# Kernel tuning notes

Hardware: AMD Instinct MI355X
Metric: run time of the kernel (lower is better)

## Reference

```python
import jax, jax.numpy as jnp
import numpy as np

HEAD_DIM = 128
N_HEADS = 32
N_KV_HEADS = 8
EPS = 1e-6
ROPE_THETA = 1e6
NEG_INF = -1e9


def _rms_norm(x, w):
    # per-head RMSNorm over last dim (head_dim), fp32 math like Qwen3RMSNorm
    xf = x.astype(jnp.float32)
    var = jnp.mean(xf * xf, axis=-1, keepdims=True)
    return (w * (xf * jax.lax.rsqrt(var + EPS))).astype(x.dtype)


def _rope_cos_sin(position_ids, dtype):
    # default rope: inv_freq = theta^(-2i/d), emb = cat(freqs, freqs)
    inv_freq = 1.0 / (ROPE_THETA ** (jnp.arange(0, HEAD_DIM, 2, dtype=jnp.float32) / HEAD_DIM))
    freqs = position_ids.astype(jnp.float32)[:, :, None] * inv_freq[None, None, :]  # [B,S,hd/2]
    emb = jnp.concatenate([freqs, freqs], axis=-1)  # [B,S,hd]
    return jnp.cos(emb).astype(dtype), jnp.sin(emb).astype(dtype)


def _rotate_half(x):
    x1, x2 = jnp.split(x, 2, axis=-1)
    return jnp.concatenate([-x2, x1], axis=-1)


def setup_inputs() -> dict:
    key = jax.random.key(0)
    ks = jax.random.split(key, 6)
    B, S, H = 1, 2048, 4096
    return {
        "hidden_states": jax.random.normal(ks[0], (B, S, H), jnp.float32),
        "position_ids": jnp.broadcast_to(jnp.arange(S, dtype=jnp.int32)[None, :], (B, S)),
        "Wq": jax.random.normal(ks[1], (N_HEADS * HEAD_DIM, H), jnp.float32) * 0.02,
        "Wk": jax.random.normal(ks[2], (N_KV_HEADS * HEAD_DIM, H), jnp.float32) * 0.02,
        "Wv": jax.random.normal(ks[3], (N_KV_HEADS * HEAD_DIM, H), jnp.float32) * 0.02,
        "Wo": jax.random.normal(ks[4], (H, N_HEADS * HEAD_DIM), jnp.float32) * 0.02,
        "q_norm_w": jnp.ones((HEAD_DIM,), jnp.float32),
        "k_norm_w": jnp.ones((HEAD_DIM,), jnp.float32),
    }


def reference(hidden_states, position_ids, Wq, Wk, Wv, Wo, q_norm_w, k_norm_w):
    B, S, H = hidden_states.shape
    scaling = HEAD_DIM ** -0.5
    n_rep = N_HEADS // N_KV_HEADS

    # projections (torch Linear: y = x @ W.T), reshape to [B, heads, S, hd]
    q = jnp.einsum('bsh,dh->bsd', hidden_states, Wq).reshape(B, S, N_HEADS, HEAD_DIM)
    k = jnp.einsum('bsh,dh->bsd', hidden_states, Wk).reshape(B, S, N_KV_HEADS, HEAD_DIM)
    v = jnp.einsum('bsh,dh->bsd', hidden_states, Wv).reshape(B, S, N_KV_HEADS, HEAD_DIM)

    q = _rms_norm(q, q_norm_w).transpose(0, 2, 1, 3)  # [B,nH,S,hd]
    k = _rms_norm(k, k_norm_w).transpose(0, 2, 1, 3)  # [B,nKV,S,hd]
    v = v.transpose(0, 2, 1, 3)

    cos, sin = _rope_cos_sin(position_ids, hidden_states.dtype)
    cos = cos[:, None, :, :]  # unsqueeze head dim
    sin = sin[:, None, :, :]
    q = q * cos + _rotate_half(q) * sin
    k = k * cos + _rotate_half(k) * sin

    # GQA repeat_kv
    k = jnp.repeat(k, n_rep, axis=1)
    v = jnp.repeat(v, n_rep, axis=1)

    scores = jnp.einsum('bhqd,bhkd->bhqk', q, k) * scaling
    causal = jnp.where(
        jnp.arange(S)[:, None] >= jnp.arange(S)[None, :], 0.0, NEG_INF
    ).astype(scores.dtype)
    scores = scores + causal[None, None, :, :]
    attn = jax.nn.softmax(scores.astype(jnp.float32), axis=-1).astype(q.dtype)

    out = jnp.einsum('bhqk,bhkd->bhqd', attn, v)
    out = out.transpose(0, 2, 1, 3).reshape(B, S, N_HEADS * HEAD_DIM)
    return jnp.einsum('bsd,hd->bsh', out, Wo)
```

## Files before the change

### kernel.cpp

```cpp
#include <hip/hip_runtime.h>
#include <hip/hip_bf16.h>

typedef unsigned short u16;
typedef __bf16 bf16x8 __attribute__((ext_vector_type(8)));
typedef u16 u16x4 __attribute__((ext_vector_type(4)));
typedef u16 u16x8 __attribute__((ext_vector_type(8)));
typedef float f32x4 __attribute__((ext_vector_type(4)));

#define S_LEN  2048
#define HID    4096
#define NHEADS 32
#define NKV    8
#define HD     128
#define QDIM   (NHEADS*HD)
#define KVDIM  (NKV*HD)
#define NT     (S_LEN/64)

__device__ __forceinline__ u16 f2bf(float f) {
  unsigned u = __float_as_uint(f);
  u += 0x7fff + ((u >> 16) & 1);
  return (u16)(u >> 16);
}
__device__ __forceinline__ void lds_load16(const u16* g, u16* l) {
  __builtin_amdgcn_global_load_lds(
      (__attribute__((address_space(1))) void*)(g),
      (__attribute__((address_space(3))) void*)(l), 16, 0, 0);
}

__global__ __launch_bounds__(256) void f2b4(
    const float* __restrict__ s0, u16* __restrict__ d0, long n0,
    const float* __restrict__ s1, u16* __restrict__ d1, long n1,
    const float* __restrict__ s2, u16* __restrict__ d2, long n2,
    const float* __restrict__ s3, u16* __restrict__ d3, long n3)
{
  const float* s; u16* d; long n; int b0, nb;
  const int b = blockIdx.x;
  if (b < 1024)      { s=s0; d=d0; n=n0; b0=0;    nb=1024; }
  else if (b < 3072) { s=s1; d=d1; n=n1; b0=1024; nb=2048; }
  else if (b < 3584) { s=s2; d=d2; n=n2; b0=3072; nb=512;  }
  else               { s=s3; d=d3; n=n3; b0=3584; nb=512;  }
  long i = (long)(b - b0)*256 + threadIdx.x;
  const long stride = (long)nb*256;
  for (; i < n; i += stride) {
    f32x4 a = ((const f32x4*)s)[i*2];
    f32x4 c = ((const f32x4*)s)[i*2 + 1];
    u16x8 o;
    #pragma unroll
    for (int j = 0; j < 4; ++j) { o[j] = f2bf(a[j]); o[4+j] = f2bf(c[j]); }
    ((u16x8*)d)[i] = o;
  }
}

__global__ __launch_bounds__(256) void f2b(
    const float* __restrict__ in, u16* __restrict__ out, long n8)
{
  long i = (long)blockIdx.x * blockDim.x + threadIdx.x;
  const long stride = (long)gridDim.x * blockDim.x;
  for (; i < n8; i += stride) {
    f32x4 a = ((const f32x4*)in)[i*2];
    f32x4 b = ((const f32x4*)in)[i*2 + 1];
    u16x8 o;
    #pragma unroll
    for (int j = 0; j < 4; ++j) { o[j] = f2bf(a[j]); o[4+j] = f2bf(b[j]); }
    ((u16x8*)out)[i] = o;
  }
}

__global__ __launch_bounds__(512, 2) void gemmQ(
    const u16* __restrict__ A, const u16* __restrict__ B,
    u16* __restrict__ Cq, u16* __restrict__ Ck, u16* __restrict__ Cv,
    int K)
{
  __shared__ u16 lds[57344];
  const int tid  = threadIdx.x;
  const int lane = tid & 63;
  const int w    = tid >> 6;
  const int wr   = w >> 2, wc = w & 3;
  const int l16  = lane & 15, lhi = lane >> 4;
  const long arow0 = (long)blockIdx.y * 256;
  const long brow0 = (long)blockIdx.x * 192;
  const int ntiles = K >> 6;

  const int cu = ((lane & 7) ^ (lane >> 3)) * 8;
  const int wl = w*8 + (lane >> 3);
  const u16* Ag[4];
  #pragma unroll
  for (int r = 0; r < 4; ++r)
    Ag[r] = A + (arow0 + r*64 + wl)*(long)K + cu;
  const u16* Bg[3];
  #pragma unroll
  for (int r = 0; r < 2; ++r) {
    const int rp = r*64 + wl;
    Bg[r] = B + (brow0 + (rp >> 5)*48 + (rp & 31))*(long)K + cu;
  }
  Bg[2] = B + (brow0 + (wl >> 4)*48 + 32 + (wl & 15))*(long)K + cu;

  auto stageA = [&](int s, int kt) {
    u16* d = lds + ((kt & 1) << 14) + w*512;
    lds_load16(Ag[s]   + (long)kt*64, d + s*4096);
    lds_load16(Ag[s+2] + (long)kt*64, d + (s+2)*4096);
  };
  auto stageB0 = [&](int kt) {
    u16* d = lds + 32768 + (kt & 1)*12288 + w*512;
    lds_load16(Bg[0] + (long)kt*64, d);
    lds_load16(Bg[1] + (long)kt*64, d + 4096);
  };
  auto stageB1 = [&](int kt) {
    u16* d = lds + 32768 + (kt & 1)*12288 + w*512;
    lds_load16(Bg[2] + (long)kt*64, d + 8192);
  };

  const int xr = (l16 & 7) << 3;
  int offA[4][2], offB[2][2], offB2[2];
  #pragma unroll
  for (int m2 = 0; m2 < 4; ++m2)
    #pragma unroll
    for (int ks = 0; ks < 2; ++ks)
      offA[m2][ks] = (wr*128 + m2*16 + l16)*64 + ((ks*32 + lhi*8) ^ xr);
  #pragma unroll
  for (int n2 = 0; n2 < 2; ++n2)
    #pragma unroll
    for (int ks = 0; ks < 2; ++ks)
      offB[n2][ks] = (wc*32 + n2*16 + l16)*64 + ((ks*32 + lhi*8) ^ xr);
  #pragma unroll
  for (int ks = 0; ks < 2; ++ks)
    offB2[ks] = 8192 + (wc*16 + l16)*64 + ((ks*32 + lhi*8) ^ xr);

  f32x4 acc[8][3] = {};

  stageA(0, 0); stageB0(0); stageB1(0); stageA(1, 0);
  stageA(0, 1); stageB0(1); stageB1(1);
  asm volatile("s_waitcnt vmcnt(5)" ::: "memory");
  __builtin_amdgcn_s_barrier();

  #pragma unroll 2
  for (int t = 0; t < ntiles; ++t) {
    const int Ab = (t & 1) << 14;
    const int Bb = 32768 + (t & 1)*12288;
    bf16x8 af[4][2], af2[4][2], bf[2][2], bf2[2];

    #pragma unroll
    for (int m2 = 0; m2 < 4; ++m2)
      #pragma unroll
      for (int ks = 0; ks < 2; ++ks)
        af[m2][ks] = *(const bf16x8*)(lds + Ab + offA[m2][ks]);
    #pragma unroll
    for (int n2 = 0; n2 < 2; ++n2)
      #pragma unroll
      for (int ks = 0; ks < 2; ++ks)
        bf[n2][ks] = *(const bf16x8*)(lds + Bb + offB[n2][ks]);
    if (t + 1 < ntiles) stageA(1, t + 1);
    __builtin_amdgcn_s_barrier();
    asm volatile("s_waitcnt lgkmcnt(0)" ::: "memory");
    __builtin_amdgcn_s_setprio(1);
    #pragma unroll
    for (int m2 = 0; m2 < 4; ++m2)
      #pragma unroll
      for (int n2 = 0; n2 < 2; ++n2)
        #pragma unroll
        for (int ks = 0; ks < 2; ++ks)
          acc[m2][n2] = __builtin_amdgcn_mfma_f32_16x16x32_bf16(
              af[m2][ks], bf[n2][ks], acc[m2][n2], 0, 0, 0);
    __builtin_amdgcn_s_setprio(0);
    __builtin_amdgcn_s_barrier();

    #pragma unroll
    for (int ks = 0; ks < 2; ++ks)
      bf2[ks] = *(const bf16x8*)(lds + Bb + offB2[ks]);
    if (t + 2 < ntiles) stageA(0, t + 2);
    __builtin_amdgcn_s_barrier();
    asm volatile("s_waitcnt lgkmcnt(0)" ::: "memory");
    __builtin_amdgcn_s_setprio(1);
    #pragma unroll
    for (int m2 = 0; m2 < 4; ++m2)
      #pragma unroll
      for (int ks = 0; ks < 2; ++ks)
        acc[m2][2] = __builtin_amdgcn_mfma_f32_16x16x32_bf16(
            af[m2][ks], bf2[ks], acc[m2][2], 0, 0, 0);
    __builtin_amdgcn_s_setprio(0);
    __builtin_amdgcn_s_barrier();

    #pragma unroll
    for (int m2 = 0; m2 < 4; ++m2)
      #pragma unroll
      for (int ks = 0; ks < 2; ++ks)
        af2[m2][ks] = *(const bf16x8*)(lds + Ab + 4096 + offA[m2][ks]);
    if (t + 2 < ntiles) stageB0(t + 2);
    __builtin_amdgcn_s_barrier();
    asm volatile("s_waitcnt lgkmcnt(0)" ::: "memory");
    __builtin_amdgcn_s_setprio(1);
    #pragma unroll
    for (int m2 = 0; m2 < 4; ++m2)
      #pragma unroll
      for (int ks = 0; ks < 2; ++ks)
        acc[4+m2][2] = __builtin_amdgcn_mfma_f32_16x16x32_bf16(
            af2[m2][ks], bf2[ks], acc[4+m2][2], 0, 0, 0);
    __builtin_amdgcn_s_setprio(0);
    __builtin_amdgcn_s_barrier();

    if (t + 2 < ntiles) stageB1(t + 2);
    __builtin_amdgcn_s_barrier();
    __builtin_amdgcn_s_setprio(1);
    #pragma unroll
    for (int m2 = 0; m2 < 4; ++m2)
      #pragma unroll
      for (int n2 = 0; n2 < 2; ++n2)
        #pragma unroll
        for (int ks = 0; ks < 2; ++ks)
          acc[4+m2][n2] = __builtin_amdgcn_mfma_f32_16x16x32_bf16(
              af2[m2][ks], bf[n2][ks], acc[4+m2][n2], 0, 0, 0);
    __builtin_amdgcn_s_setprio(0);
    if (t + 2 < ntiles) { asm volatile("s_waitcnt vmcnt(5)" ::: "memory"); }
    else                { asm volatile("s_waitcnt vmcnt(0)" ::: "memory"); }
    __builtin_amdgcn_s_barrier();
  }

  #pragma unroll
  for (int m = 0; m < 8; ++m) {
    const long row = arow0 + wr*128 + (m >> 2)*64 + (m & 3)*16 + lhi*4;
    #pragma unroll
    for (int n = 0; n < 3; ++n) {
      const long col = brow0 + wc*48 + n*16 + l16;
      if (col < QDIM) {
        #pragma unroll
        for (int r = 0; r < 4; ++r)
          Cq[(row + r)*QDIM + col] = f2bf(acc[m][n][r]);
      } else if (col < QDIM + KVDIM) {
        #pragma unroll
        for (int r = 0; r < 4; ++r)
          Ck[(row + r)*KVDIM + (col - QDIM)] = f2bf(acc[m][n][r]);
      } else {
        u16x4 o;
        #pragma unroll
        for (int r = 0; r < 4; ++r) o[r] = f2bf(acc[m][n][r]);
        *(u16x4*)(Cv + (col - QDIM - KVDIM)*(long)S_LEN + row) = o;
      }
    }
  }
}

__global__ __launch_bounds__(512, 2) void gemmF(
    const u16* __restrict__ A, const u16* __restrict__ B,
    float* __restrict__ C, int M, int N, int K)
{
  __shared__ u16 lds[49152];
  const int tid  = threadIdx.x;
  const int lane = tid & 63;
  const int w    = tid >> 6;
  const int wr   = w >> 2, wc = w & 3;
  const int l16  = lane & 15, lhi = lane >> 4;
  const long arow0 = (long)blockIdx.y * 128;
  const long brow0 = (long)blockIdx.x * 256;
  const int ntiles = K >> 6;

  const int cu = ((lane & 7) ^ (lane >> 3)) * 8;
  const int rA  = (w >> 2)*64 + (w & 3)*8;
  const int rB1c = 128 + (w >> 2)*64 + (w & 3)*8;
  const u16* srcA  = A + (arow0 + rA   + (lane >> 3))*(long)K + cu;
  const u16* srcB0 = B + (brow0 + rA   + (lane >> 3))*(long)K + cu;
  const u16* srcB1 = B + (brow0 + rB1c + (lane >> 3))*(long)K + cu;
  u16* const dA  = lds + rA*64;
  u16* const dB0 = lds + 16384 + rA*64;
  u16* const dB1 = lds + 16384 + rB1c*64;

  auto stageA = [&](int s, int kt) {
    lds_load16(srcA + (long)(s*32)*K + kt*64,
               dA + ((kt & 1) << 13) + s*2048);
  };
  auto stageB = [&](int s, int kt) {
    const long so = (long)(s*32)*K + kt*64;
    const int  d  = ((kt & 1) << 14) + s*2048;
    lds_load16(srcB0 + so, dB0 + d);
    lds_load16(srcB1 + so, dB1 + d);
  };

  const int xr = (l16 & 7) << 3;
  int offA[2][2], offB[2][2];
  #pragma unroll
  for (int m = 0; m < 2; ++m)
    #pragma unroll
    for (int ks = 0; ks < 2; ++ks)
      offA[m][ks] = (wr*64 + m*16 + l16)*64 + ((ks*32 + lhi*8) ^ xr);
  #pragma unroll
  for (int n = 0; n < 2; ++n)
    #pragma unroll
    for (int ks = 0; ks < 2; ++ks)
      offB[n][ks] = (wc*64 + n*16 + l16)*64 + ((ks*32 + lhi*8) ^ xr);

  f32x4 acc[4][4] = {};

  stageA(0, 0); stageA(1, 0); stageB(0, 0); stageB(1, 0);
  if (ntiles > 1) { stageA(0, 1); stageB(0, 1); stageB(1, 1); }
  asm volatile("s_waitcnt vmcnt(5)" ::: "memory");
  __builtin_amdgcn_s_barrier();

  #pragma unroll 2
  for (int t = 0; t < ntiles; ++t) {
    const int Ab = (t & 1) << 13;
    const int Bb = 16384 + ((t & 1) << 14);
    bf16x8 af[2][2], bf[2][2], af2[2][2], bf2[2][2];

    #pragma unroll
    for (int m = 0; m < 2; ++m)
      #pragma unroll
      for (int ks = 0; ks < 2; ++ks)
        af[m][ks] = *(const bf16x8*)(lds + Ab + offA[m][ks]);
    #pragma unroll
    for (int n = 0; n < 2; ++n)
      #pragma unroll
      for (int ks = 0; ks < 2; ++ks)
        bf[n][ks] = *(const bf16x8*)(lds + Bb + offB[n][ks]);
    if (t + 1 < ntiles) stageA(1, t + 1);
    __builtin_amdgcn_s_barrier();
    asm volatile("s_waitcnt lgkmcnt(0)" ::: "memory");
    __builtin_amdgcn_s_setprio(1);
    #pragma unroll
    for (int m = 0; m < 2; ++m)
      #pragma unroll
      for (int n = 0; n < 2; ++n)
        #pragma unroll
        for (int ks = 0; ks < 2; ++ks)
          acc[m][n] = __builtin_amdgcn_mfma_f32_16x16x32_bf16(
              af[m][ks], bf[n][ks], acc[m][n], 0, 0, 0);
    __builtin_amdgcn_s_setprio(0);
    __builtin_amdgcn_s_barrier();

    #pragma unroll
    for (int n = 0; n < 2; ++n)
      #pragma unroll
      for (int ks = 0; ks < 2; ++ks)
        bf2[n][ks] = *(const bf16x8*)(lds + Bb + 2048 + offB[n][ks]);
    if (t + 2 < ntiles) stageA(0, t + 2);
    __builtin_amdgcn_s_barrier();
    asm volatile("s_waitcnt lgkmcnt(0)" ::: "memory");
    __builtin_amdgcn_s_setprio(1);
    #pragma unroll
    for (int m = 0; m < 2; ++m)
      #pragma unroll
      for (int n = 0; n < 2; ++n)
        #pragma unroll
        for (int ks = 0; ks < 2; ++ks)
          acc[m][2+n] = __builtin_amdgcn_mfma_f32_16x16x32_bf16(
              af[m][ks], bf2[n][ks], acc[m][2+n], 0, 0, 0);
    __builtin_amdgcn_s_setprio(0);
    __builtin_amdgcn_s_barrier();

    #pragma unroll
    for (int m = 0; m < 2; ++m)
      #pragma unroll
      for (int ks = 0; ks < 2; ++ks)
        af2[m][ks] = *(const bf16x8*)(lds + Ab + 2048 + offA[m][ks]);
    if (t + 2 < ntiles) stageB(0, t + 2);
    __builtin_amdgcn_s_barrier();
    asm volatile("s_waitcnt lgkmcnt(0)" ::: "memory");
    __builtin_amdgcn_s_setprio(1);
    #pragma unroll
    for (int m = 0; m < 2; ++m)
      #pragma unroll
      for (int n = 0; n < 2; ++n)
        #pragma unroll
        for (int ks = 0; ks < 2; ++ks)
          acc[2+m][2+n] = __builtin_amdgcn_mfma_f32_16x16x32_bf16(
              af2[m][ks], bf2[n][ks], acc[2+m][2+n], 0, 0, 0);
    __builtin_amdgcn_s_setprio(0);
    __builtin_amdgcn_s_barrier();

    if (t + 2 < ntiles) stageB(1, t + 2);
    __builtin_amdgcn_s_barrier();
    __builtin_amdgcn_s_setprio(1);
    #pragma unroll
    for (int m = 0; m < 2; ++m)
      #pragma unroll
      for (int n = 0; n < 2; ++n)
        #pragma unroll
        for (int ks = 0; ks < 2; ++ks)
          acc[2+m][n] = __builtin_amdgcn_mfma_f32_16x16x32_bf16(
              af2[m][ks], bf[n][ks], acc[2+m][n], 0, 0, 0);
    __builtin_amdgcn_s_setprio(0);
    if (t + 2 < ntiles) { asm volatile("s_waitcnt vmcnt(5)" ::: "memory"); }
    else                { asm volatile("s_waitcnt vmcnt(0)" ::: "memory"); }
    __builtin_amdgcn_s_barrier();
  }

  #pragma unroll
  for (int mi = 0; mi < 4; ++mi) {
    const long row = arow0 + wr*64 + (mi >> 1)*32 + (mi & 1)*16 + lhi*4;
    #pragma unroll
    for (int ni = 0; ni < 4; ++ni) {
      const long col = brow0 + wc*64 + (ni >> 1)*32 + (ni & 1)*16 + l16;
      #pragma unroll
      for (int r = 0; r < 4; ++r)
        C[(row + r)*N + col] = acc[mi][ni][r];
    }
  }
}

__global__ __launch_bounds__(256) void norm_rope2(
    u16* __restrict__ Qb, u16* __restrict__ Kb,
    const float* __restrict__ qw, const float* __restrict__ kw,
    const int* __restrict__ pos)
{
  const int row  = blockIdx.x * 4 + (threadIdx.x >> 6);
  const int lane = threadIdx.x & 63;
  u16* p; const float* nw; float sc; int s;
  if (row < S_LEN*NHEADS) {
    p = Qb + (long)row * HD; nw = qw; sc = 0.08838834764831845f; s = row >> 5;
  } else {
    const int r2 = row - S_LEN*NHEADS;
    p = Kb + (long)r2 * HD; nw = kw; sc = 1.0f; s = r2 >> 3;
  }

  float x1 = __uint_as_float(((unsigned)p[lane]) << 16);
  float x2 = __uint_as_float(((unsigned)p[lane + 64]) << 16);
  float ss = x1*x1 + x2*x2;
  #pragma unroll
  for (int m = 32; m >= 1; m >>= 1) ss += __shfl_xor(ss, m);
  const float inv = rsqrtf(ss * (1.0f/128.0f) + 1e-6f);
  x1 *= inv * nw[lane];
  x2 *= inv * nw[lane + 64];

  const float inv_freq = expf(-(float)lane * (13.815510557964274f / 64.0f));
  const float ang = (float)pos[s] * inv_freq;
  float sn, cs;
  sincosf(ang, &sn, &cs);
  p[lane]      = f2bf((x1*cs - x2*sn) * sc);
  p[lane + 64] = f2bf((x2*cs + x1*sn) * sc);
}

__global__ __launch_bounds__(256, 4) void attn(
    const u16* __restrict__ Q, const u16* __restrict__ K,
    const u16* __restrict__ VT, u16* __restrict__ O,
    float* __restrict__ OP0, float* __restrict__ OP1, float* __restrict__ ML)
{
  __shared__ u16 Ks[64*128];
  __shared__ u16 Vt[128*64];
  __shared__ u16 Ps[4*16*64];

  const int tid  = threadIdx.x;
  const int lane = tid & 63;
  const int w    = tid >> 6;
  const int l16  = lane & 15, lhi = lane >> 4;

  const int bx = blockIdx.x;
  int h, Tq, t0, t1;
  bool split;
  if (bx < 1024) {
    const int pid  = bx >> 1;
    const int half = bx & 1;
    Tq = 31 - (pid >> 5);
    h  = pid & 31;
    const int nk = Tq + 1, nh = nk >> 1;
    t0 = half ? nh : 0;
    t1 = half ? nk : nh;
    split = true;
  } else {
    const int s = bx - 1024;
    Tq = 15 - (s >> 5);
    h  = s & 31;
    t0 = 0; t1 = Tq + 1;
    split = false;
  }
  const int kh = h >> 2;
  const int qrow0 = Tq*64 + w*16;

  bf16x8 qf[4];
  #pragma unroll
  for (int ks = 0; ks < 4; ++ks)
    qf[ks] = *(const bf16x8*)(Q + (long)(qrow0 + l16)*QDIM + h*HD + ks*32 + lhi*8);

  float mr[4] = {-1e30f,-1e30f,-1e30f,-1e30f};
  float lr[4] = {0.f,0.f,0.f,0.f};
  f32x4 of[8] = {};
  u16* Pw = Ps + w*16*64;

  for (int t = t0; t < t1; ++t) {
    const int kv0 = t * 64;
    #pragma unroll
    for (int i = 0; i < 4; ++i) {
      const int r   = w*16 + i*4 + lhi;
      const int col = (l16*8) ^ ((r & 7) << 3);
      lds_load16(K + (long)(kv0 + r)*KVDIM + kh*HD + col,
                 Ks + (w*16 + i*4)*128);
    }
    #pragma unroll
    for (int i = 0; i < 4; ++i) {
      const int r   = w*32 + i*8 + (lane >> 3);
      const int col = ((lane & 7)*8) ^ ((r & 7) << 3);
      lds_load16(VT + (long)(kh*HD + r)*S_LEN + kv0 + col,
                 Vt + (w*32 + i*8)*64);
    }
    __syncthreads();

    f32x4 sa[4] = {};
    __builtin_amdgcn_s_setprio(1);
    #pragma unroll
    for (int n = 0; n < 4; ++n)
      #pragma unroll
      for (int ks = 0; ks < 4; ++ks) {
        bf16x8 kf = *(const bf16x8*)(
            Ks + (n*16 + l16)*128 + ((ks*32 + lhi*8) ^ ((l16 & 7) << 3)));
        sa[n] = __builtin_amdgcn_mfma_f32_16x16x32_bf16(qf[ks], kf, sa[n], 0, 0, 0);
      }
    __builtin_amdgcn_s_setprio(0);

    const bool diag = (t == Tq);
    float pm[4];
    #pragma unroll
    for (int r = 0; r < 4; ++r) {
      const int grow = qrow0 + lhi*4 + r;
      #pragma unroll
      for (int n = 0; n < 4; ++n) {
        float sv = sa[n][r];
        if (diag && (kv0 + n*16 + l16 > grow)) sv = -1e9f;
        sa[n][r] = sv;
      }
      float p01 = fmaxf(sa[0][r], sa[1][r]);
      float p23 = fmaxf(sa[2][r], sa[3][r]);
      float pmx = fmaxf(p01, p23);
      pmx = fmaxf(pmx, __shfl_xor(pmx, 1));
      pmx = fmaxf(pmx, __shfl_xor(pmx, 2));
      pmx = fmaxf(pmx, __shfl_xor(pmx, 4));
      pmx = fmaxf(pmx, __shfl_xor(pmx, 8));
      pm[r] = pmx;
    }
    bool need = (pm[0] > mr[0] + 8.f) | (pm[1] > mr[1] + 8.f) |
                (pm[2] > mr[2] + 8.f) | (pm[3] > mr[3] + 8.f);
    if (__any(need)) {
      #pragma unroll
      for (int r = 0; r < 4; ++r) {
        const float mnew  = fmaxf(mr[r], pm[r]);
        const float alpha = __expf(mr[r] - mnew);
        mr[r] = mnew;
        lr[r] *= alpha;
        #pragma unroll
        for (int c = 0; c < 8; ++c) of[c][r] *= alpha;
      }
    }
    #pragma unroll
    for (int r = 0; r < 4; ++r) {
      float rsum = 0.f;
      #pragma unroll
      for (int n = 0; n < 4; ++n) {
        float pv = __expf(sa[n][r] - mr[r]);
        sa[n][r] = pv;
        rsum += pv;
      }
      rsum += __shfl_xor(rsum, 1);
      rsum += __shfl_xor(rsum, 2);
      rsum += __shfl_xor(rsum, 4);
      rsum += __shfl_xor(rsum, 8);
      lr[r] += rsum;
    }

    #pragma unroll
    for (int r = 0; r < 4; ++r) {
      const int prow = lhi*4 + r;
      #pragma unroll
      for (int n = 0; n < 4; ++n)
        Pw[prow*64 + ((n*16 + l16) ^ ((prow & 7) << 3))] = f2bf(sa[n][r]);
    }
    __builtin_amdgcn_s_setprio(1);
    #pragma unroll
    for (int ks = 0; ks < 2; ++ks) {
      bf16x8 pf = *(const bf16x8*)(
          Pw + l16*64 + ((ks*32 + lhi*8) ^ ((l16 & 7) << 3)));
      #pragma unroll
      for (int c = 0; c < 8; ++c) {
        bf16x8 vf = *(const bf16x8*)(
            Vt + (c*16 + l16)*64 + ((ks*32 + lhi*8) ^ ((l16 & 7) << 3)));
        of[c] = __builtin_amdgcn_mfma_f32_16x16x32_bf16(pf, vf, of[c], 0, 0, 0);
      }
    }
    __builtin_amdgcn_s_setprio(0);
    __syncthreads();
  }

  if (split) {
    float* Op = ((bx & 1) ? OP1 : OP0) + (long)(bx >> 1) * 8192;
    #pragma unroll
    for (int r = 0; r < 4; ++r) {
      const int row = w*16 + lhi*4 + r;
      #pragma unroll
      for (int c = 0; c < 8; ++c)
        Op[row*128 + c*16 + l16] = of[c][r];
      if (l16 == 0) {
        ML[(long)bx*128 + row*2]     = mr[r];
        ML[(long)bx*128 + row*2 + 1] = lr[r];
      }
    }
  } else {
    #pragma unroll
    for (int r = 0; r < 4; ++r) {
      const float invl = 1.0f / lr[r];
      const long orow = (long)(qrow0 + lhi*4 + r) * QDIM + h*HD;
      #pragma unroll
      for (int c = 0; c < 8; ++c)
        O[orow + c*16 + l16] = f2bf(of[c][r] * invl);
    }
  }
}

__global__ __launch_bounds__(256) void mrg(
    const float* __restrict__ OP0, const float* __restrict__ OP1,
    const float* __restrict__ ML, u16* __restrict__ O)
{
  const int r0  = blockIdx.x*2 + (threadIdx.x >> 7);
  const int pid = r0 >> 6;
  const int row = r0 & 63;
  const int d   = threadIdx.x & 127;
  const int Tq  = 31 - (pid >> 5);
  const int h   = pid & 31;
  const long mb0 = (long)(2*pid)*128 + row*2;
  const long mb1 = mb0 + 128;
  const float m0 = ML[mb0],     l0 = ML[mb0 + 1];
  const float m1 = ML[mb1],     l1 = ML[mb1 + 1];
  const float m  = fmaxf(m0, m1);
  const float a0 = __expf(m0 - m), a1 = __expf(m1 - m);
  const float o0 = OP0[(long)pid*8192 + row*128 + d];
  const float o1 = OP1[(long)pid*8192 + row*128 + d];
  const float o  = (o0*a0 + o1*a1) / (l0*a0 + l1*a1);
  O[(long)(Tq*64 + row)*QDIM + h*HD + d] = f2bf(o);
}

extern "C" void kernel_launch(void* const* d_in, const int* in_sizes, int n_in,
                              void* d_out, int out_size, void* d_ws, size_t ws_size,
                              hipStream_t stream) {
  (void)in_sizes; (void)n_in; (void)out_size; (void)ws_size;
  const float* hs  = (const float*)d_in[0];
  const int*   pos = (const int*)d_in[1];
  const float* Wq  = (const float*)d_in[2];
  const float* Wk  = (const float*)d_in[3];
  const float* Wv  = (const float*)d_in[4];
  const float* Wo  = (const float*)d_in[5];
  const float* qw  = (const float*)d_in[6];
  const float* kw  = (const float*)d_in[7];

  u16* hsB = (u16*)d_ws;
  u16* W1  = hsB + (long)S_LEN*HID;
  u16* WkB = W1  + (long)QDIM*HID;
  u16* WvB = WkB + (long)KVDIM*HID;
  u16* Kb  = WvB + (long)KVDIM*HID;
  u16* VT  = Kb  + (long)S_LEN*KVDIM;
  u16* AO  = VT  + (long)KVDIM*S_LEN;
  u16* Qb  = (u16*)d_out;

  float* OP0 = (float*)hsB;
  float* OP1 = (float*)WkB;
  float* ML  = (float*)(Qb + (long)S_LEN*QDIM);

  f2b4<<<4096, 256, 0, stream>>>(hs, hsB, (long)S_LEN*HID/8,
                                 Wq, W1,  (long)QDIM*HID/8,
                                 Wk, WkB, (long)KVDIM*HID/8,
                                 Wv, WvB, (long)KVDIM*HID/8);

  gemmQ<<<dim3((QDIM+2*KVDIM)/192, S_LEN/256), 512, 0, stream>>>(
      hsB, W1, Qb, Kb, VT, HID);

  norm_rope2<<<(S_LEN*NHEADS + S_LEN*NKV)/4, 256, 0, stream>>>(
      Qb, Kb, qw, kw, pos);

  f2b<<<2048, 256, 0, stream>>>(Wo, W1, (long)HID*QDIM/8);

  attn<<<dim3(1536), 256, 0, stream>>>(Qb, Kb, VT, AO, OP0, OP1, ML);
  mrg<<<dim3(16384), 256, 0, stream>>>(OP0, OP1, ML, AO);

  gemmF<<<dim3(HID/256, S_LEN/128), 512, 0, stream>>>(
      AO, W1, (float*)d_out, S_LEN, HID, QDIM);
}
```

Baseline: 361.1 us.

## Balance causal attention work by pairing high and low query tiles per block

After: 348.7 us. 1.04x faster.

```diff
diff --git a/kernel.cpp b/kernel.cpp
--- a/kernel.cpp
+++ b/kernel.cpp
@@ -441,161 +441,158 @@
   const int w    = tid >> 6;
   const int l16  = lane & 15, lhi = lane >> 4;
 
-  const int bx = blockIdx.x;
-  int h, Tq, t0, t1;
-  bool split;
-  if (bx < 1024) {
-    const int pid  = bx >> 1;
-    const int half = bx & 1;
-    Tq = 31 - (pid >> 5);
-    h  = pid & 31;
-    const int nk = Tq + 1, nh = nk >> 1;
-    t0 = half ? nh : 0;
-    t1 = half ? nk : nh;
-    split = true;
-  } else {
-    const int s = bx - 1024;
-    Tq = 15 - (s >> 5);
-    h  = s & 31;
-    t0 = 0; t1 = Tq + 1;
-    split = false;
-  }
-  const int kh = h >> 2;
-  const int qrow0 = Tq*64 + w*16;
-
-  bf16x8 qf[4];
-  #pragma unroll
-  for (int ks = 0; ks < 4; ++ks)
-    qf[ks] = *(const bf16x8*)(Q + (long)(qrow0 + l16)*QDIM + h*HD + ks*32 + lhi*8);
-
-  float mr[4] = {-1e30f,-1e30f,-1e30f,-1e30f};
-  float lr[4] = {0.f,0.f,0.f,0.f};
-  f32x4 of[8] = {};
-  u16* Pw = Ps + w*16*64;
-
-  for (int t = t0; t < t1; ++t) {
-    const int kv0 = t * 64;
-    #pragma unroll
-    for (int i = 0; i < 4; ++i) {
-      const int r   = w*16 + i*4 + lhi;
-      const int col = (l16*8) ^ ((r & 7) << 3);
-      lds_load16(K + (long)(kv0 + r)*KVDIM + kh*HD + col,
-                 Ks + (w*16 + i*4)*128);
+  const int kh   = blockIdx.x & 7;
+  const int idx  = blockIdx.x >> 3;
+  const int cc   = idx & 31;
+  const int jj   = idx >> 5;
+  const int h    = kh*4 + jj;
+  const int k    = cc ^ (jj & 1);
+  const int p    = k >> 1;
+  const int role = k & 1;
+  const int hi   = 31 - p, lo = p;
+  const int pid  = h*16 + p;
+
+  const int nseg = role ? 2 : 1;
+  for (int sg = 0; sg < nseg; ++sg) {
+    const int qt  = sg ? lo : hi;
+    const int tt0 = (sg == 0 && role) ? 16 : 0;
+    const int tt1 = sg ? (lo + 1) : (role ? hi + 1 : 16);
+    const int qrow0 = qt*64 + w*16;
+
+    bf16x8 qf[4];
+    #pragma unroll
+    for (int ks = 0; ks < 4; ++ks)
+      qf[ks] = *(const bf16x8*)(Q + (long)(qrow0 + l16)*QDIM + h*HD + ks*32 + lhi*8);
+
+    float mr[4] = {-1e30f,-1e30f,-1e30f,-1e30f};
+    float lr[4] = {0.f,0.f,0.f,0.f};
+    f32x4 of[8] = {};
+    u16* Pw = Ps + w*16*64;
+
+    for (int t = tt0; t < tt1; ++t) {
+      const int kv0 = t * 64;
+      #pragma unroll
+      for (int i = 0; i < 4; ++i) {
+        const int r   = w*16 + i*4 + lhi;
+        const int col = (l16*8) ^ ((r & 7) << 3);
+        lds_load16(K + (long)(kv0 + r)*KVDIM + kh*HD + col,
+                   Ks + (w*16 + i*4)*128);
+      }
+      #pragma unroll
+      for (int i = 0; i < 4; ++i) {
+        const int r   = w*32 + i*8 + (lane >> 3);
+        const int col = ((lane & 7)*8) ^ ((r & 7) << 3);
+        lds_load16(VT + (long)(kh*HD + r)*S_LEN + kv0 + col,
+                   Vt + (w*32 + i*8)*64);
+      }
+      __syncthreads();
+
+      f32x4 sa[4] = {};
+      __builtin_amdgcn_s_setprio(1);
+      #pragma unroll
+      for (int n = 0; n < 4; ++n)
+        #pragma unroll
+        for (int ks = 0; ks < 4; ++ks) {
+          bf16x8 kf = *(const bf16x8*)(
+              Ks + (n*16 + l16)*128 + ((ks*32 + lhi*8) ^ ((l16 & 7) << 3)));
+          sa[n] = __builtin_amdgcn_mfma_f32_16x16x32_bf16(qf[ks], kf, sa[n], 0, 0, 0);
+        }
+      __builtin_amdgcn_s_setprio(0);
+
+      const bool diag = (t == qt);
+      float pm[4];
+      #pragma unroll
+      for (int r = 0; r < 4; ++r) {
+        const int grow = qrow0 + lhi*4 + r;
+        #pragma unroll
+        for (int n = 0; n < 4; ++n) {
+          float sv = sa[n][r];
+          if (diag && (kv0 + n*16 + l16 > grow)) sv = -1e9f;
+          sa[n][r] = sv;
+        }
+        float p01 = fmaxf(sa[0][r], sa[1][r]);
+        float p23 = fmaxf(sa[2][r], sa[3][r]);
+        float pmx = fmaxf(p01, p23);
+        pmx = fmaxf(pmx, __shfl_xor(pmx, 1));
+        pmx = fmaxf(pmx, __shfl_xor(pmx, 2));
+        pmx = fmaxf(pmx, __shfl_xor(pmx, 4));
+        pmx = fmaxf(pmx, __shfl_xor(pmx, 8));
+        pm[r] = pmx;
+      }
+      bool need = (pm[0] > mr[0] + 8.f) | (pm[1] > mr[1] + 8.f) |
+                  (pm[2] > mr[2] + 8.f) | (pm[3] > mr[3] + 8.f);
+      if (__any(need)) {
+        #pragma unroll
+        for (int r = 0; r < 4; ++r) {
+          const float mnew  = fmaxf(mr[r], pm[r]);
+          const float alpha = __expf(mr[r] - mnew);
+          mr[r] = mnew;
+          lr[r] *= alpha;
+          #pragma unroll
+          for (int c = 0; c < 8; ++c) of[c][r] *= alpha;
+        }
+      }
+      #pragma unroll
+      for (int r = 0; r < 4; ++r) {
+        float rsum = 0.f;
+        #pragma unroll
+        for (int n = 0; n < 4; ++n) {
+          float pv = __expf(sa[n][r] - mr[r]);
+          sa[n][r] = pv;
+          rsum += pv;
+        }
+        rsum += __shfl_xor(rsum, 1);
+        rsum += __shfl_xor(rsum, 2);
+        rsum += __shfl_xor(rsum, 4);
+        rsum += __shfl_xor(rsum, 8);
+        lr[r] += rsum;
+      }
+
+      #pragma unroll
+      for (int r = 0; r < 4; ++r) {
+        const int prow = lhi*4 + r;
+        #pragma unroll
+        for (int n = 0; n < 4; ++n)
+          Pw[prow*64 + ((n*16 + l16) ^ ((prow & 7) << 3))] = f2bf(sa[n][r]);
+      }
+      __builtin_amdgcn_s_setprio(1);
+      #pragma unroll
+      for (int ks = 0; ks < 2; ++ks) {
+        bf16x8 pf = *(const bf16x8*)(
+            Pw + l16*64 + ((ks*32 + lhi*8) ^ ((l16 & 7) << 3)));
+        #pragma unroll
+        for (int c = 0; c < 8; ++c) {
+          bf16x8 vf = *(const bf16x8*)(
+              Vt + (c*16 + l16)*64 + ((ks*32 + lhi*8) ^ ((l16 & 7) << 3)));
+          of[c] = __builtin_amdgcn_mfma_f32_16x16x32_bf16(pf, vf, of[c], 0, 0, 0);
+        }
+      }
+      __builtin_amdgcn_s_setprio(0);
+      __syncthreads();
     }
-    #pragma unroll
-    for (int i = 0; i < 4; ++i) {
-      const int r   = w*32 + i*8 + (lane >> 3);
-      const int col = ((lane & 7)*8) ^ ((r & 7) << 3);
-      lds_load16(VT + (long)(kh*HD + r)*S_LEN + kv0 + col,
-                 Vt + (w*32 + i*8)*64);
-    }
-    __syncthreads();
-
-    f32x4 sa[4] = {};
-    __builtin_amdgcn_s_setprio(1);
-    #pragma unroll
-    for (int n = 0; n < 4; ++n)
-      #pragma unroll
-      for (int ks = 0; ks < 4; ++ks) {
-        bf16x8 kf = *(const bf16x8*)(
-            Ks + (n*16 + l16)*128 + ((ks*32 + lhi*8) ^ ((l16 & 7) << 3)));
-        sa[n] = __builtin_amdgcn_mfma_f32_16x16x32_bf16(qf[ks], kf, sa[n], 0, 0, 0);
-      }
-    __builtin_amdgcn_s_setprio(0);
-
-    const bool diag = (t == Tq);
-    float pm[4];
-    #pragma unroll
-    for (int r = 0; r < 4; ++r) {
-      const int grow = qrow0 + lhi*4 + r;
-      #pragma unroll
-      for (int n = 0; n < 4; ++n) {
-        float sv = sa[n][r];
-        if (diag && (kv0 + n*16 + l16 > grow)) sv = -1e9f;
-        sa[n][r] = sv;
-      }
-      float p01 = fmaxf(sa[0][r], sa[1][r]);
-      float p23 = fmaxf(sa[2][r], sa[3][r]);
-      float pmx = fmaxf(p01, p23);
-      pmx = fmaxf(pmx, __shfl_xor(pmx, 1));
-      pmx = fmaxf(pmx, __shfl_xor(pmx, 2));
-      pmx = fmaxf(pmx, __shfl_xor(pmx, 4));
-      pmx = fmaxf(pmx, __shfl_xor(pmx, 8));
-      pm[r] = pmx;
-    }
-    bool need = (pm[0] > mr[0] + 8.f) | (pm[1] > mr[1] + 8.f) |
-                (pm[2] > mr[2] + 8.f) | (pm[3] > mr[3] + 8.f);
-    if (__any(need)) {
+
+    if (sg == 0) {
+      float* Op = (role ? OP1 : OP0) + (long)pid * 8192;
       #pragma unroll
       for (int r = 0; r < 4; ++r) {
-        const float mnew  = fmaxf(mr[r], pm[r]);
-        const float alpha = __expf(mr[r] - mnew);
-        mr[r] = mnew;
-        lr[r] *= alpha;
-        #pragma unroll
-        for (int c = 0; c < 8; ++c) of[c][r] *= alpha;
-      }
-    }
-    #pragma unroll
-    for (int r = 0; r < 4; ++r) {
-      float rsum = 0.f;
-      #pragma unroll
-      for (int n = 0; n < 4; ++n) {
-        float pv = __expf(sa[n][r] - mr[r]);
-        sa[n][r] = pv;
-        rsum += pv;
-      }
-      rsum += __shfl_xor(rsum, 1);
-      rsum += __shfl_xor(rsum, 2);
-      rsum += __shfl_xor(rsum, 4);
-      rsum += __shfl_xor(rsum, 8);
-      lr[r] += rsum;
-    }
-
-    #pragma unroll
-    for (int r = 0; r < 4; ++r) {
-      const int prow = lhi*4 + r;
-      #pragma unroll
-      for (int n = 0; n < 4; ++n)
-        Pw[prow*64 + ((n*16 + l16) ^ ((prow & 7) << 3))] = f2bf(sa[n][r]);
-    }
-    __builtin_amdgcn_s_setprio(1);
-    #pragma unroll
-    for (int ks = 0; ks < 2; ++ks) {
-      bf16x8 pf = *(const bf16x8*)(
-          Pw + l16*64 + ((ks*32 + lhi*8) ^ ((l16 & 7) << 3)));
-      #pragma unroll
-      for (int c = 0; c < 8; ++c) {
-        bf16x8 vf = *(const bf16x8*)(
-            Vt + (c*16 + l16)*64 + ((ks*32 + lhi*8) ^ ((l16 & 7) << 3)));
-        of[c] = __builtin_amdgcn_mfma_f32_16x16x32_bf16(pf, vf, of[c], 0, 0, 0);
-      }
-    }
-    __builtin_amdgcn_s_setprio(0);
-    __syncthreads();
-  }
-
-  if (split) {
-    float* Op = ((bx & 1) ? OP1 : OP0) + (long)(bx >> 1) * 8192;
-    #pragma unroll
-    for (int r = 0; r < 4; ++r) {
-      const int row = w*16 + lhi*4 + r;
-      #pragma unroll
-      for (int c = 0; c < 8; ++c)
-        Op[row*128 + c*16 + l16] = of[c][r];
-      if (l16 == 0) {
-        ML[(long)bx*128 + row*2]     = mr[r];
-        ML[(long)bx*128 + row*2 + 1] = lr[r];
-      }
-    }
-  } else {
-    #pragma unroll
-    for (int r = 0; r < 4; ++r) {
-      const float invl = 1.0f / lr[r];
-      const long orow = (long)(qrow0 + lhi*4 + r) * QDIM + h*HD;
-      #pragma unroll
-      for (int c = 0; c < 8; ++c)
-        O[orow + c*16 + l16] = f2bf(of[c][r] * invl);
+        const int row = w*16 + lhi*4 + r;
+        #pragma unroll
+        for (int c = 0; c < 8; ++c)
+          Op[row*128 + c*16 + l16] = of[c][r];
+        if (l16 == 0) {
+          ML[((long)pid*2 + role)*128 + row*2]     = mr[r];
+          ML[((long)pid*2 + role)*128 + row*2 + 1] = lr[r];
+        }
+      }
+    } else {
+      #pragma unroll
+      for (int r = 0; r < 4; ++r) {
+        const float invl = 1.0f / lr[r];
+        const long orow = (long)(qrow0 + lhi*4 + r) * QDIM + h*HD;
+        #pragma unroll
+        for (int c = 0; c < 8; ++c)
+          O[orow + c*16 + l16] = f2bf(of[c][r] * invl);
+      }
     }
   }
 }
@@ -608,9 +605,9 @@
   const int pid = r0 >> 6;
   const int row = r0 & 63;
   const int d   = threadIdx.x & 127;
-  const int Tq  = 31 - (pid >> 5);
-  const int h   = pid & 31;
-  const long mb0 = (long)(2*pid)*128 + row*2;
+  const int h   = pid >> 4;
+  const int Tq  = 31 - (pid & 15);
+  const long mb0 = ((long)pid*2)*128 + row*2;
   const long mb1 = mb0 + 128;
   const float m0 = ML[mb0],     l0 = ML[mb0 + 1];
   const float m1 = ML[mb1],     l1 = ML[mb1 + 1];
@@ -661,7 +658,7 @@
 
   f2b<<<2048, 256, 0, stream>>>(Wo, W1, (long)HID*QDIM/8);
 
-  attn<<<dim3(1536), 256, 0, stream>>>(Qb, Kb, VT, AO, OP0, OP1, ML);
+  attn<<<dim3(1024), 256, 0, stream>>>(Qb, Kb, VT, AO, OP0, OP1, ML);
   mrg<<<dim3(16384), 256, 0, stream>>>(OP0, OP1, ML, AO);
 
   gemmF<<<dim3(HID/256, S_LEN/128), 512, 0, stream>>>(
```
